# Kernel tuning notes

Hardware: AMD Instinct MI355X
Metric: run time of the kernel (lower is better)

## Reference

```python
import jax, jax.numpy as jnp
import numpy as np

EMBED_DIM = 1024
BATCH, SEQ = 4, 2048


def setup_inputs() -> dict:
    key = jax.random.key(0)
    kx, kq, kk, kv = jax.random.split(key, 4)
    return {
        "x": jax.random.normal(kx, (BATCH, SEQ, EMBED_DIM), dtype=jnp.float32),
        "q_weight": jax.random.normal(kq, (EMBED_DIM, EMBED_DIM), dtype=jnp.float32),
        "k_weight": jax.random.normal(kk, (EMBED_DIM, EMBED_DIM), dtype=jnp.float32),
        "v_weight": jax.random.normal(kv, (EMBED_DIM, EMBED_DIM), dtype=jnp.float32),
    }


def reference(x, q_weight, k_weight, v_weight):
    # x: [b, s, d]
    d = x.shape[-1]
    Q = jnp.einsum('bsd,de->bse', x, q_weight)
    K = jnp.einsum('bsd,de->bse', x, k_weight)
    V = jnp.einsum('bsd,de->bse', x, v_weight)
    scores = jnp.einsum('bqe,bke->bqk', Q, K) / jnp.sqrt(jnp.float32(d))
    attn = jax.nn.softmax(scores, axis=-1)
    out = jnp.einsum('bqk,bke->bqe', attn, V)
    return out
```

## Files before the change

kernel.cpp:

```cpp
#include <hip/hip_runtime.h>
#include <hip/hip_bf16.h>


typedef _Float16 half8 __attribute__((ext_vector_type(8)));
typedef _Float16 half4v __attribute__((ext_vector_type(4)));
typedef float f32x4 __attribute__((ext_vector_type(4)));

#define GLOBAL_AS __attribute__((address_space(1)))
#define LDS_AS __attribute__((address_space(3)))

__device__ __forceinline__ void gll16(const _Float16* g, _Float16* l) {
    __builtin_amdgcn_global_load_lds((GLOBAL_AS const void*)g, (LDS_AS void*)l, 16, 0, 0);
}

template <int NPROD, int OUTMODE>
__global__ __launch_bounds__(256) void gemm_nt(
    const _Float16* __restrict__ A0, const _Float16* __restrict__ A1,
    const _Float16* __restrict__ B0, const _Float16* __restrict__ B1,
    float* __restrict__ Cf, _Float16* __restrict__ C0, _Float16* __restrict__ C1,
    int lda, int ldb, int ldc, int K,
    long sA, long sB, long sC, float scale, float scale2) {
    constexpr int NTILES = (NPROD == 3) ? 4 : 2;
    __shared__ alignas(16) _Float16 smem[NTILES * 4096];
    _Float16* sA0 = smem;
    _Float16* sB0 = smem + 4096;
    _Float16* sA1 = (NPROD == 3) ? smem + 8192 : smem;
    _Float16* sB1 = (NPROD == 3) ? smem + 12288 : smem;

    const int tid = threadIdx.x;
    const int wave = tid >> 6, lane = tid & 63;
    const int wm = (wave >> 1) * 64, wn = (wave & 1) * 64;
    const int quad = lane >> 4, r16 = lane & 15;

    const long zA = (long)blockIdx.z * sA;
    const long zB = (long)blockIdx.z * sB;
    const long zC = (long)blockIdx.z * sC;

    const float sc = (blockIdx.y * 2 < gridDim.y) ? scale : scale2;

    const int trow = tid >> 2;
    const int tcol = ((((tid & 3) - ((tid >> 3) & 3)) & 3)) * 8;
    const _Float16* gA0 = A0 + zA + (long)(blockIdx.x * 128 + trow) * lda + tcol;
    const _Float16* gB0 = B0 + zB + (long)(blockIdx.y * 128 + trow) * ldb + tcol;
    const _Float16* gA1 = (NPROD == 3) ? (A1 + zA + (long)(blockIdx.x * 128 + trow) * lda + tcol) : nullptr;
    const _Float16* gB1 = (NPROD == 3) ? (B1 + zB + (long)(blockIdx.y * 128 + trow) * ldb + tcol) : nullptr;

    f32x4 acc[4][4];
#pragma unroll
    for (int i = 0; i < 4; ++i)
#pragma unroll
        for (int j = 0; j < 4; ++j) {
            acc[i][j][0] = 0.f; acc[i][j][1] = 0.f; acc[i][j][2] = 0.f; acc[i][j][3] = 0.f;
        }

    const int ldsoff = tid * 8;
    const int p8 = ((quad + (r16 >> 1)) & 3) * 8;

    for (int k0 = 0; k0 < K; k0 += 32) {
        __syncthreads();
        gll16(gA0, sA0 + ldsoff);
        gll16(gA0 + 64 * lda, sA0 + ldsoff + 2048);
        gll16(gB0, sB0 + ldsoff);
        gll16(gB0 + 64 * ldb, sB0 + ldsoff + 2048);
        if (NPROD == 3) {
            gll16(gA1, sA1 + ldsoff);
            gll16(gA1 + 64 * lda, sA1 + ldsoff + 2048);
            gll16(gB1, sB1 + ldsoff);
            gll16(gB1 + 64 * ldb, sB1 + ldsoff + 2048);
        }
        gA0 += 32; gB0 += 32;
        if (NPROD == 3) { gA1 += 32; gB1 += 32; }
        __syncthreads();

        half8 a0[4], b0[4], a1[4], b1[4];
#pragma unroll
        for (int i = 0; i < 4; ++i) {
            a0[i] = *(const half8*)(sA0 + (wm + i * 16 + r16) * 32 + p8);
            b0[i] = *(const half8*)(sB0 + (wn + i * 16 + r16) * 32 + p8);
            if (NPROD == 3) {
                a1[i] = *(const half8*)(sA1 + (wm + i * 16 + r16) * 32 + p8);
                b1[i] = *(const half8*)(sB1 + (wn + i * 16 + r16) * 32 + p8);
            }
        }
#pragma unroll
        for (int i = 0; i < 4; ++i)
#pragma unroll
            for (int j = 0; j < 4; ++j) {
                acc[i][j] = __builtin_amdgcn_mfma_f32_16x16x32_f16(a0[i], b0[j], acc[i][j], 0, 0, 0);
                if (NPROD == 3) {
                    acc[i][j] = __builtin_amdgcn_mfma_f32_16x16x32_f16(a0[i], b1[j], acc[i][j], 0, 0, 0);
                    acc[i][j] = __builtin_amdgcn_mfma_f32_16x16x32_f16(a1[i], b0[j], acc[i][j], 0, 0, 0);
                }
            }
    }

    const int crow0 = blockIdx.x * 128 + wm + quad * 4;
    const int ccol0 = blockIdx.y * 128 + wn + r16;
#pragma unroll
    for (int i = 0; i < 4; ++i)
#pragma unroll
        for (int j = 0; j < 4; ++j)
#pragma unroll
            for (int r = 0; r < 4; ++r) {
                long off = zC + (long)(crow0 + i * 16 + r) * ldc + (ccol0 + j * 16);
                float v = acc[i][j][r] * sc;
                if (OUTMODE == 0) {
                    Cf[off] = v;
                } else if (OUTMODE == 2) {
                    C0[off] = (_Float16)v;
                } else {
                    _Float16 h = (_Float16)v;
                    C0[off] = h;
                    C1[off] = (_Float16)(v - (float)h);
                }
            }
}

__global__ __launch_bounds__(256) void split_x(const float* __restrict__ in,
                                               _Float16* __restrict__ o0,
                                               _Float16* __restrict__ o1, long n4) {
    long i = (long)blockIdx.x * 256 + threadIdx.x;
    if (i >= n4) return;
    float4 v = ((const float4*)in)[i];
    float a[4] = {v.x, v.y, v.z, v.w};
    half4v h, l;
#pragma unroll
    for (int c = 0; c < 4; ++c) {
        h[c] = (_Float16)a[c];
        l[c] = (_Float16)(a[c] - (float)h[c]);
    }
    ((half4v*)o0)[i] = h;
    ((half4v*)o1)[i] = l;
}

__global__ __launch_bounds__(256) void transpose_split_w3(
    const float* __restrict__ wq, const float* __restrict__ wk,
    const float* __restrict__ wv,
    _Float16* __restrict__ qk0, _Float16* __restrict__ qk1,
    _Float16* __restrict__ v0, _Float16* __restrict__ v1) {
    const int z = blockIdx.z;
    const float* in = (z == 0) ? wq : (z == 1) ? wk : wv;
    _Float16* o0 = (z == 0) ? qk0 : (z == 1) ? qk0 + 1024 * 1024 : v0;
    _Float16* o1 = (z == 0) ? qk1 : (z == 1) ? qk1 + 1024 * 1024 : v1;

    __shared__ float t[32][33];
    const int c0 = blockIdx.x * 32, r0 = blockIdx.y * 32;
    const int tx = threadIdx.x & 31, ty = threadIdx.x >> 5;
#pragma unroll
    for (int i = 0; i < 32; i += 8)
        t[ty + i][tx] = in[(long)(r0 + ty + i) * 1024 + c0 + tx];
    __syncthreads();
#pragma unroll
    for (int i = 0; i < 32; i += 8) {
        float v = t[tx][ty + i];
        _Float16 h = (_Float16)v;
        long o = (long)(c0 + ty + i) * 1024 + r0 + tx;
        o0[o] = h;
        o1[o] = (_Float16)(v - (float)h);
    }
}

__global__ __launch_bounds__(256) void softmax_rows(const float* __restrict__ S,
                                                    _Float16* __restrict__ P) {
    const int n = 2048;
    const long base = (long)blockIdx.x * n;
    const float4* row4 = (const float4*)(S + base);
    const int tid = threadIdx.x;
    const int wave = tid >> 6;

    float4 v0 = row4[tid * 2];
    float4 v1 = row4[tid * 2 + 1];
    float v[8] = {v0.x, v0.y, v0.z, v0.w, v1.x, v1.y, v1.z, v1.w};
    float lm = -3.4e38f;
#pragma unroll
    for (int t = 0; t < 8; ++t) lm = fmaxf(lm, v[t]);
#pragma unroll
    for (int o = 32; o > 0; o >>= 1) lm = fmaxf(lm, __shfl_xor(lm, o));
    __shared__ float redm[4];
    __shared__ float reds[4];
    if ((tid & 63) == 0) redm[wave] = lm;
    __syncthreads();
    lm = fmaxf(fmaxf(redm[0], redm[1]), fmaxf(redm[2], redm[3]));

    float e[8];
    float ls = 0.f;
#pragma unroll
    for (int t = 0; t < 8; ++t) {
        e[t] = __expf(v[t] - lm);
        ls += e[t];
    }
#pragma unroll
    for (int o = 32; o > 0; o >>= 1) ls += __shfl_xor(ls, o);
    if ((tid & 63) == 0) reds[wave] = ls;
    __syncthreads();
    ls = reds[0] + reds[1] + reds[2] + reds[3];
    const float inv = 1.f / ls;
    half8 p;
#pragma unroll
    for (int t = 0; t < 8; ++t) p[t] = (_Float16)(e[t] * inv);
    ((half8*)(P + base))[tid] = p;
}

extern "C" void kernel_launch(void* const* d_in, const int* in_sizes, int n_in,
                              void* d_out, int out_size, void* d_ws, size_t ws_size,
                              hipStream_t stream) {
    (void)in_sizes; (void)n_in; (void)out_size; (void)ws_size;
    const float* x = (const float*)d_in[0];
    const float* wq = (const float*)d_in[1];
    const float* wk = (const float*)d_in[2];
    const float* wv = (const float*)d_in[3];
    float* out = (float*)d_out;
    char* ws = (char*)d_ws;

    const long MB = 1l << 20;
    _Float16* Wqk0 = (_Float16*)(ws + 0 * MB);
    _Float16* Wqk1 = (_Float16*)(ws + 4 * MB);
    _Float16* Wv0  = (_Float16*)(ws + 8 * MB);
    _Float16* Wv1  = (_Float16*)(ws + 10 * MB);
    _Float16* x0   = (_Float16*)(ws + 12 * MB);
    _Float16* x1   = (_Float16*)(ws + 28 * MB);
    _Float16* P    = (_Float16*)(ws + 12 * MB);
    _Float16* QK0  = (_Float16*)(ws + 44 * MB);
    _Float16* QK1  = (_Float16*)(ws + 76 * MB);
    _Float16* Vt   = (_Float16*)(ws + 108 * MB);
    float*    S    = (float*)(ws + 124 * MB);

    const int B = 4, SEQ = 2048, D = 1024;
    const long M = (long)B * SEQ;
    const long ssq = (long)SEQ * SEQ;

    split_x<<<dim3((M * D / 4 + 255) / 256), dim3(256), 0, stream>>>(x, x0, x1, M * D / 4);

    transpose_split_w3<<<dim3(32, 32, 3), dim3(256), 0, stream>>>(
        wq, wk, wv, Wqk0, Wqk1, Wv0, Wv1);

    gemm_nt<3, 1><<<dim3(64, 16, 1), dim3(256), 0, stream>>>(
        x0, x1, Wqk0, Wqk1, nullptr, QK0, QK1, D, D, 2 * D, D,
        0, 0, 0, 0.03125f, 1.0f);

    gemm_nt<1, 2><<<dim3(8, 64, 1), dim3(256), 0, stream>>>(
        Wv0, nullptr, x0, nullptr, nullptr, Vt, nullptr, D, D, (int)M, D,
        0, 0, 0, 1.0f, 1.0f);

    gemm_nt<3, 0><<<dim3(16, 16, B), dim3(256), 0, stream>>>(
        QK0, QK1, QK0 + D, QK1 + D, S, nullptr, nullptr, 2 * D, 2 * D, SEQ, D,
        (long)SEQ * 2 * D, (long)SEQ * 2 * D, ssq, 1.0f, 1.0f);

    softmax_rows<<<dim3(B * SEQ), dim3(256), 0, stream>>>(S, P);

    gemm_nt<1, 0><<<dim3(16, 8, B), dim3(256), 0, stream>>>(
        P, nullptr, Vt, nullptr, out, nullptr, nullptr, SEQ, (int)M, D, SEQ,
        ssq, (long)SEQ, (long)SEQ * D, 1.0f, 1.0f);
}
```

Baseline: 429.0 us.

## Switch GEMMs to 32x32x16 MFMA and fuse prep kernels into one launch

New measurement: 445.4 us. 3.8% more time.

```diff
diff --git a/kernel.cpp b/kernel.cpp
--- a/kernel.cpp
+++ b/kernel.cpp
@@ -4,7 +4,7 @@
 
 typedef _Float16 half8 __attribute__((ext_vector_type(8)));
 typedef _Float16 half4v __attribute__((ext_vector_type(4)));
-typedef float f32x4 __attribute__((ext_vector_type(4)));
+typedef float f32x16 __attribute__((ext_vector_type(16)));
 
 #define GLOBAL_AS __attribute__((address_space(1)))
 #define LDS_AS __attribute__((address_space(3)))
@@ -30,7 +30,7 @@
     const int tid = threadIdx.x;
     const int wave = tid >> 6, lane = tid & 63;
     const int wm = (wave >> 1) * 64, wn = (wave & 1) * 64;
-    const int quad = lane >> 4, r16 = lane & 15;
+    const int q2 = lane >> 5, r32 = lane & 31;
 
     const long zA = (long)blockIdx.z * sA;
     const long zB = (long)blockIdx.z * sB;
@@ -45,16 +45,18 @@
     const _Float16* gA1 = (NPROD == 3) ? (A1 + zA + (long)(blockIdx.x * 128 + trow) * lda + tcol) : nullptr;
     const _Float16* gB1 = (NPROD == 3) ? (B1 + zB + (long)(blockIdx.y * 128 + trow) * ldb + tcol) : nullptr;
 
-    f32x4 acc[4][4];
-#pragma unroll
-    for (int i = 0; i < 4; ++i)
-#pragma unroll
-        for (int j = 0; j < 4; ++j) {
-            acc[i][j][0] = 0.f; acc[i][j][1] = 0.f; acc[i][j][2] = 0.f; acc[i][j][3] = 0.f;
-        }
+    f32x16 acc[2][2];
+#pragma unroll
+    for (int i = 0; i < 2; ++i)
+#pragma unroll
+        for (int j = 0; j < 2; ++j)
+#pragma unroll
+            for (int r = 0; r < 16; ++r) acc[i][j][r] = 0.f;
 
     const int ldsoff = tid * 8;
-    const int p8 = ((quad + (r16 >> 1)) & 3) * 8;
+    int p8[2];
+#pragma unroll
+    for (int h = 0; h < 2; ++h) p8[h] = (((q2 + 2 * h) + (r32 >> 1)) & 3) * 8;
 
     for (int k0 = 0; k0 < K; k0 += 32) {
         __syncthreads();
@@ -72,37 +74,42 @@
         if (NPROD == 3) { gA1 += 32; gB1 += 32; }
         __syncthreads();
 
-        half8 a0[4], b0[4], a1[4], b1[4];
-#pragma unroll
-        for (int i = 0; i < 4; ++i) {
-            a0[i] = *(const half8*)(sA0 + (wm + i * 16 + r16) * 32 + p8);
-            b0[i] = *(const half8*)(sB0 + (wn + i * 16 + r16) * 32 + p8);
-            if (NPROD == 3) {
-                a1[i] = *(const half8*)(sA1 + (wm + i * 16 + r16) * 32 + p8);
-                b1[i] = *(const half8*)(sB1 + (wn + i * 16 + r16) * 32 + p8);
-            }
-        }
-#pragma unroll
-        for (int i = 0; i < 4; ++i)
-#pragma unroll
-            for (int j = 0; j < 4; ++j) {
-                acc[i][j] = __builtin_amdgcn_mfma_f32_16x16x32_f16(a0[i], b0[j], acc[i][j], 0, 0, 0);
+        half8 a0[2][2], b0[2][2], a1[2][2], b1[2][2];
+#pragma unroll
+        for (int i = 0; i < 2; ++i)
+#pragma unroll
+            for (int h = 0; h < 2; ++h) {
+                a0[i][h] = *(const half8*)(sA0 + (wm + i * 32 + r32) * 32 + p8[h]);
+                b0[i][h] = *(const half8*)(sB0 + (wn + i * 32 + r32) * 32 + p8[h]);
                 if (NPROD == 3) {
-                    acc[i][j] = __builtin_amdgcn_mfma_f32_16x16x32_f16(a0[i], b1[j], acc[i][j], 0, 0, 0);
-                    acc[i][j] = __builtin_amdgcn_mfma_f32_16x16x32_f16(a1[i], b0[j], acc[i][j], 0, 0, 0);
+                    a1[i][h] = *(const half8*)(sA1 + (wm + i * 32 + r32) * 32 + p8[h]);
+                    b1[i][h] = *(const half8*)(sB1 + (wn + i * 32 + r32) * 32 + p8[h]);
                 }
             }
-    }
-
-    const int crow0 = blockIdx.x * 128 + wm + quad * 4;
-    const int ccol0 = blockIdx.y * 128 + wn + r16;
-#pragma unroll
-    for (int i = 0; i < 4; ++i)
-#pragma unroll
-        for (int j = 0; j < 4; ++j)
-#pragma unroll
-            for (int r = 0; r < 4; ++r) {
-                long off = zC + (long)(crow0 + i * 16 + r) * ldc + (ccol0 + j * 16);
+#pragma unroll
+        for (int i = 0; i < 2; ++i)
+#pragma unroll
+            for (int j = 0; j < 2; ++j)
+#pragma unroll
+                for (int h = 0; h < 2; ++h) {
+                    acc[i][j] = __builtin_amdgcn_mfma_f32_32x32x16_f16(a0[i][h], b0[j][h], acc[i][j], 0, 0, 0);
+                    if (NPROD == 3) {
+                        acc[i][j] = __builtin_amdgcn_mfma_f32_32x32x16_f16(a0[i][h], b1[j][h], acc[i][j], 0, 0, 0);
+                        acc[i][j] = __builtin_amdgcn_mfma_f32_32x32x16_f16(a1[i][h], b0[j][h], acc[i][j], 0, 0, 0);
+                    }
+                }
+    }
+
+    const int crow0 = blockIdx.x * 128 + wm + 4 * q2;
+    const int ccol0 = blockIdx.y * 128 + wn + r32;
+#pragma unroll
+    for (int i = 0; i < 2; ++i)
+#pragma unroll
+        for (int j = 0; j < 2; ++j)
+#pragma unroll
+            for (int r = 0; r < 16; ++r) {
+                int row = crow0 + i * 32 + (r & 3) + 8 * (r >> 2);
+                long off = zC + (long)row * ldc + (ccol0 + j * 32);
                 float v = acc[i][j][r] * sc;
                 if (OUTMODE == 0) {
                     Cf[off] = v;
@@ -116,35 +123,37 @@
             }
 }
 
-__global__ __launch_bounds__(256) void split_x(const float* __restrict__ in,
-                                               _Float16* __restrict__ o0,
-                                               _Float16* __restrict__ o1, long n4) {
-    long i = (long)blockIdx.x * 256 + threadIdx.x;
-    if (i >= n4) return;
-    float4 v = ((const float4*)in)[i];
-    float a[4] = {v.x, v.y, v.z, v.w};
-    half4v h, l;
-#pragma unroll
-    for (int c = 0; c < 4; ++c) {
-        h[c] = (_Float16)a[c];
-        l[c] = (_Float16)(a[c] - (float)h[c]);
-    }
-    ((half4v*)o0)[i] = h;
-    ((half4v*)o1)[i] = l;
-}
-
-__global__ __launch_bounds__(256) void transpose_split_w3(
+__global__ __launch_bounds__(256) void prep_fused(
+    const float* __restrict__ x, _Float16* __restrict__ x0, _Float16* __restrict__ x1,
+    long n4, int nsplit,
     const float* __restrict__ wq, const float* __restrict__ wk,
     const float* __restrict__ wv,
     _Float16* __restrict__ qk0, _Float16* __restrict__ qk1,
     _Float16* __restrict__ v0, _Float16* __restrict__ v1) {
-    const int z = blockIdx.z;
+    __shared__ float t[32][33];
+    if ((int)blockIdx.x < nsplit) {
+        long i = (long)blockIdx.x * 256 + threadIdx.x;
+        if (i >= n4) return;
+        float4 v = ((const float4*)x)[i];
+        float a[4] = {v.x, v.y, v.z, v.w};
+        half4v h, l;
+#pragma unroll
+        for (int c = 0; c < 4; ++c) {
+            h[c] = (_Float16)a[c];
+            l[c] = (_Float16)(a[c] - (float)h[c]);
+        }
+        ((half4v*)x0)[i] = h;
+        ((half4v*)x1)[i] = l;
+        return;
+    }
+    const int idx = blockIdx.x - nsplit;
+    const int z = idx >> 10;
+    const int tile = idx & 1023;
     const float* in = (z == 0) ? wq : (z == 1) ? wk : wv;
     _Float16* o0 = (z == 0) ? qk0 : (z == 1) ? qk0 + 1024 * 1024 : v0;
     _Float16* o1 = (z == 0) ? qk1 : (z == 1) ? qk1 + 1024 * 1024 : v1;
 
-    __shared__ float t[32][33];
-    const int c0 = blockIdx.x * 32, r0 = blockIdx.y * 32;
+    const int c0 = (tile & 31) * 32, r0 = (tile >> 5) * 32;
     const int tx = threadIdx.x & 31, ty = threadIdx.x >> 5;
 #pragma unroll
     for (int i = 0; i < 32; i += 8)
@@ -228,11 +237,10 @@
     const int B = 4, SEQ = 2048, D = 1024;
     const long M = (long)B * SEQ;
     const long ssq = (long)SEQ * SEQ;
-
-    split_x<<<dim3((M * D / 4 + 255) / 256), dim3(256), 0, stream>>>(x, x0, x1, M * D / 4);
-
-    transpose_split_w3<<<dim3(32, 32, 3), dim3(256), 0, stream>>>(
-        wq, wk, wv, Wqk0, Wqk1, Wv0, Wv1);
+    const int nsplit = (int)((M * D / 4 + 255) / 256);
+
+    prep_fused<<<dim3(nsplit + 3072), dim3(256), 0, stream>>>(
+        x, x0, x1, M * D / 4, nsplit, wq, wk, wv, Wqk0, Wqk1, Wv0, Wv1);
 
     gemm_nt<3, 1><<<dim3(64, 16, 1), dim3(256), 0, stream>>>(
         x0, x1, Wqk0, Wqk1, nullptr, QK0, QK1, D, D, 2 * D, D,
```
